# Kernel tuning notes

Hardware: AMD Instinct MI355X
Metric: run time of the kernel (lower is better)

## Reference

```python
import jax, jax.numpy as jnp
import numpy as np

B, L, D = 128, 1024, 2048

def setup_inputs() -> dict:
    key = jax.random.key(0)
    k1, k2 = jax.random.split(key)
    features = jax.random.normal(k1, (B, L, D), dtype=jnp.float32)
    lengths = jax.random.randint(k2, (B,), 0, L, dtype=jnp.int32)
    return {"features": features, "lengths": lengths}

def reference(features, lengths):
    # Prefix mean over seq axis; lengths<=0 falls back to full-sequence mean.
    Lq = features.shape[1]
    eff_len = jnp.where(lengths > 0, lengths, Lq)  # [B]
    mask = (jnp.arange(Lq)[None, :] < eff_len[:, None]).astype(features.dtype)  # [B, L]
    summed = jnp.einsum('bld,bl->bd', features, mask)  # [B, D]
    pooled = summed / eff_len[:, None].astype(features.dtype)
    return pooled
```

## Files before the change

### kernel.cpp

```cpp
#include <hip/hip_runtime.h>

constexpr int Bc = 128;
constexpr int Lc = 1024;
constexpr int Dc = 2048;

constexpr int THREADS   = 256;
constexpr int VEC       = 4;
constexpr int DCOLS_BLK = THREADS * VEC;
constexpr int DBLKS     = Dc / DCOLS_BLK;
constexpr int NL        = 8;

typedef float v4f __attribute__((ext_vector_type(4)));

__global__ __launch_bounds__(THREADS) void avg_pool_var_kernel(
    const float* __restrict__ feat,
    const int*   __restrict__ lengths,
    float*       __restrict__ out)
{
    int bid  = blockIdx.x;
    int lc   = bid % NL;
    int dblk = (bid / NL) % DBLKS;
    int b    = bid / (NL * DBLKS);

    int len = lengths[b];
    int eff = (len > 0) ? len : Lc;

    int col = dblk * DCOLS_BLK + (int)threadIdx.x * VEC;
    const float* p = feat + (size_t)b * Lc * Dc + (size_t)lc * Dc + col;

    float ax = 0.f, ay = 0.f, az = 0.f, aw = 0.f;
    #pragma unroll 4
    for (int l = lc; l < eff; l += NL, p += (size_t)NL * Dc) {
        v4f v = __builtin_nontemporal_load(reinterpret_cast<const v4f*>(p));
        ax += v.x; ay += v.y; az += v.z; aw += v.w;
    }

    float inv = 1.0f / (float)eff;
    float* o = out + (size_t)b * Dc + col;
    atomicAdd(o + 0, ax * inv);
    atomicAdd(o + 1, ay * inv);
    atomicAdd(o + 2, az * inv);
    atomicAdd(o + 3, aw * inv);
}

extern "C" void kernel_launch(void* const* d_in, const int* in_sizes, int n_in,
                              void* d_out, int out_size, void* d_ws, size_t ws_size,
                              hipStream_t stream)
{
    const float* feat    = (const float*)d_in[0];
    const int*   lengths = (const int*)d_in[1];
    float*       out     = (float*)d_out;

    (void)hipMemsetAsync(out, 0, (size_t)out_size * sizeof(float), stream);

    dim3 grid(Bc * DBLKS * NL);
    dim3 block(THREADS);
    avg_pool_var_kernel<<<grid, block, 0, stream>>>(feat, lengths, out);
}
```

Before: 102.7 us.

## Load-balance prefix-mean rows across a fixed grid via prefix sums over lengths

Instead of one block per (batch, D-chunk, L-phase), which leaves blocks idle or overloaded depending on each sequence's length, every block computes prefix sums of the effective lengths in shared memory. It then takes an equal slice of the flattened valid rows and walks it, flushing partial sums with atomics whenever it crosses a batch boundary. Each 512-thread block covers the full D width of 2048 floats per row. This evens out work across blocks and stops reading masked rows. The cost is a serial prefix scan per block, a binary search, and a single load chain per thread with no unrolling, which may limit memory-level parallelism.

```diff
diff --git a/kernel.cpp b/kernel.cpp
--- a/kernel.cpp
+++ b/kernel.cpp
@@ -4,11 +4,8 @@
 constexpr int Lc = 1024;
 constexpr int Dc = 2048;
 
-constexpr int THREADS   = 256;
-constexpr int VEC       = 4;
-constexpr int DCOLS_BLK = THREADS * VEC;
-constexpr int DBLKS     = Dc / DCOLS_BLK;
-constexpr int NL        = 8;
+constexpr int THREADS = 512;
+constexpr int GRID    = 1024;
 
 typedef float v4f __attribute__((ext_vector_type(4)));
 
@@ -17,30 +14,64 @@
     const int*   __restrict__ lengths,
     float*       __restrict__ out)
 {
-    int bid  = blockIdx.x;
-    int lc   = bid % NL;
-    int dblk = (bid / NL) % DBLKS;
-    int b    = bid / (NL * DBLKS);
+    __shared__ int E[Bc];
+    __shared__ int S[Bc + 1];
 
-    int len = lengths[b];
-    int eff = (len > 0) ? len : Lc;
+    int tid = threadIdx.x;
+    if (tid < Bc) {
+        int len = lengths[tid];
+        E[tid] = (len > 0) ? len : Lc;
+    }
+    __syncthreads();
+    if (tid == 0) {
+        int s = 0;
+        #pragma unroll 8
+        for (int b = 0; b < Bc; ++b) { S[b] = s; s += E[b]; }
+        S[Bc] = s;
+    }
+    __syncthreads();
 
-    int col = dblk * DCOLS_BLK + (int)threadIdx.x * VEC;
-    const float* p = feat + (size_t)b * Lc * Dc + (size_t)lc * Dc + col;
+    int total = S[Bc];
+    int r0 = (int)((long long)blockIdx.x * total / GRID);
+    int r1 = (int)((long long)(blockIdx.x + 1) * total / GRID);
+    if (r0 >= r1) return;
 
+    int lo = 0, hi = Bc - 1;
+    while (lo < hi) {
+        int mid = (lo + hi + 1) >> 1;
+        if (S[mid] <= r0) lo = mid; else hi = mid - 1;
+    }
+    int cur_b = lo;
+    int nb    = S[cur_b + 1];
+
+    int col = tid * 4;
     float ax = 0.f, ay = 0.f, az = 0.f, aw = 0.f;
-    #pragma unroll 4
-    for (int l = lc; l < eff; l += NL, p += (size_t)NL * Dc) {
+
+    for (int r = r0; r < r1; ++r) {
+        if (r >= nb) {
+            float inv = 1.0f / (float)(nb - S[cur_b]);
+            float* o = out + (size_t)cur_b * Dc + col;
+            atomicAdd(o + 0, ax * inv);
+            atomicAdd(o + 1, ay * inv);
+            atomicAdd(o + 2, az * inv);
+            atomicAdd(o + 3, aw * inv);
+            ax = ay = az = aw = 0.f;
+            while (r >= S[cur_b + 1]) ++cur_b;
+            nb = S[cur_b + 1];
+        }
+        int l = r - S[cur_b];
+        const float* p = feat + ((size_t)cur_b * Lc + l) * Dc + col;
         v4f v = __builtin_nontemporal_load(reinterpret_cast<const v4f*>(p));
         ax += v.x; ay += v.y; az += v.z; aw += v.w;
     }
-
-    float inv = 1.0f / (float)eff;
-    float* o = out + (size_t)b * Dc + col;
-    atomicAdd(o + 0, ax * inv);
-    atomicAdd(o + 1, ay * inv);
-    atomicAdd(o + 2, az * inv);
-    atomicAdd(o + 3, aw * inv);
+    {
+        float inv = 1.0f / (float)(nb - S[cur_b]);
+        float* o = out + (size_t)cur_b * Dc + col;
+        atomicAdd(o + 0, ax * inv);
+        atomicAdd(o + 1, ay * inv);
+        atomicAdd(o + 2, az * inv);
+        atomicAdd(o + 3, aw * inv);
+    }
 }
 
 extern "C" void kernel_launch(void* const* d_in, const int* in_sizes, int n_in,
@@ -53,7 +84,5 @@
 
     (void)hipMemsetAsync(out, 0, (size_t)out_size * sizeof(float), stream);
 
-    dim3 grid(Bc * DBLKS * NL);
-    dim3 block(THREADS);
-    avg_pool_var_kernel<<<grid, block, 0, stream>>>(feat, lengths, out);
+    avg_pool_var_kernel<<<dim3(GRID), dim3(THREADS), 0, stream>>>(feat, lengths, out);
 }
```

Result: slower. 108.1 us (+5.3%).
